# Kernel optimization log

Hardware: AMD Instinct MI355X
Metric: run time of the kernel (lower is better)

Reference implementation:

```python
import jax, jax.numpy as jnp
import numpy as np

N_NODES = 50000
N_EDGES = 800000
D_IN = 128
D_OUT = 128


def setup_inputs() -> dict:
    key = jax.random.key(0)
    k1, k2, k3, k4, k5 = jax.random.split(key, 5)
    gain = float(np.sqrt(2.0))  # calculate_gain('relu')
    # xavier_uniform bound: gain * sqrt(6/(fan_in+fan_out))
    bound = gain * float(np.sqrt(6.0 / (D_IN + D_OUT)))
    feat = jax.random.normal(k1, (N_NODES, D_IN), dtype=jnp.float32)
    weight = jax.random.uniform(k2, (D_IN, D_OUT), minval=-bound, maxval=bound, dtype=jnp.float32)
    loop_weight = jax.random.uniform(k3, (D_IN, D_OUT), minval=-bound, maxval=bound, dtype=jnp.float32)
    h_bias = jnp.zeros((D_OUT,), dtype=jnp.float32)
    src = jax.random.randint(k4, (N_EDGES,), 0, N_NODES, dtype=jnp.int32)
    dst = jax.random.randint(k5, (N_EDGES,), 0, N_NODES, dtype=jnp.int32)
    return {"feat": feat, "weight": weight, "h_bias": h_bias,
            "loop_weight": loop_weight, "src": src, "dst": dst}


def reference(feat, weight, h_bias, loop_weight, src, dst):
    # message: m_e = feat[src_e] @ W ; aggregate: h_v = sum_{e: dst_e=v} m_e
    # (equivalently transform-then-gather, which avoids the [E, D] matmul)
    transformed = feat @ weight                    # [N, D_out]
    msgs = transformed[src]                        # [E, D_out] gather
    h = jax.ops.segment_sum(msgs, dst, num_segments=feat.shape[0])  # [N, D_out]
    h = h + h_bias                                 # bias
    h = h + feat @ loop_weight                     # self-loop
    # activation=None, dropout=0 -> identity
    return h
```

## Files before the change

kernel.cpp:

```cpp
#include <hip/hip_runtime.h>

#define D 128
#define CAP 64
#define FCHUNK 4096

typedef __attribute__((ext_vector_type(8))) short bf16x8;
typedef __attribute__((ext_vector_type(4))) float f32x4;

__device__ inline unsigned short f2bf_rne(float x) {
    unsigned u = __float_as_uint(x);
    return (unsigned short)((u + 0x7FFFu + ((u >> 16) & 1u)) >> 16);
}

__global__ __launch_bounds__(256) void prep_kernel(
    const float* __restrict__ W, const float* __restrict__ LW,
    unsigned short* __restrict__ Bt, int* __restrict__ cursor, int ncur)
{
    int tid = blockIdx.x * 256 + threadIdx.x;
    if (tid < 2 * D * D) {
        int n = tid >> 7;
        int k = tid & 127;
        float v = (n < D) ? W[(size_t)k * D + n] : LW[(size_t)k * D + (n - D)];
        Bt[(size_t)n * D + k] = f2bf_rne(v);
    }
    int j = tid - 2 * D * D;
    if (j >= 0 && j < ncur) cursor[j] = 0;
}

__global__ __launch_bounds__(256) void fill_kernel(
    const int* __restrict__ src, const int* __restrict__ dst,
    int* __restrict__ cursor, unsigned short* __restrict__ ebuf,
    int E, int cstride)
{
    const int chunk = blockIdx.x >> 3;
    const int cls   = blockIdx.x & 7;
    const int base  = chunk * FCHUNK;

    for (int i = threadIdx.x; i < FCHUNK; i += 256) {
        const int e = base + i;
        if (e >= E) break;
        const int d = dst[e];
        const int s = src[e];
        if ((d & 7) == cls) {
            int pos = atomicAdd(&cursor[(cls * cstride) + (d >> 3)], 1);
            if (pos < CAP) ebuf[(size_t)d * CAP + pos] = (unsigned short)s;
        }
    }
}

__global__ __launch_bounds__(256) void mfma_transform(
    const float* __restrict__ feat, const unsigned short* __restrict__ Bt,
    unsigned short* __restrict__ T2, int N)
{
    const int wave = threadIdx.x >> 6;
    const int lane = threadIdx.x & 63;
    const int wrow0 = blockIdx.x * 64 + wave * 16;
    const int m    = lane & 15;
    const int kg   = lane >> 4;

    int arow_idx = wrow0 + m;
    if (arow_idx >= N) arow_idx = N - 1;
    const float* arow = feat + (size_t)arow_idx * D;

    bf16x8 a[4];
#pragma unroll
    for (int ks = 0; ks < 4; ++ks) {
        const float4 f0 = *(const float4*)(arow + ks * 32 + kg * 8);
        const float4 f1 = *(const float4*)(arow + ks * 32 + kg * 8 + 4);
        bf16x8 v;
        v[0] = (short)f2bf_rne(f0.x); v[1] = (short)f2bf_rne(f0.y);
        v[2] = (short)f2bf_rne(f0.z); v[3] = (short)f2bf_rne(f0.w);
        v[4] = (short)f2bf_rne(f1.x); v[5] = (short)f2bf_rne(f1.y);
        v[6] = (short)f2bf_rne(f1.z); v[7] = (short)f2bf_rne(f1.w);
        a[ks] = v;
    }

    f32x4 acc[16];
#pragma unroll
    for (int t = 0; t < 16; ++t) acc[t] = (f32x4){0.f, 0.f, 0.f, 0.f};

#pragma unroll
    for (int t = 0; t < 16; ++t) {
        const unsigned short* brow = Bt + (size_t)(t * 16 + m) * D;
        bf16x8 b0 = *(const bf16x8*)(brow + 0 * 32 + kg * 8);
        bf16x8 b1 = *(const bf16x8*)(brow + 1 * 32 + kg * 8);
        bf16x8 b2 = *(const bf16x8*)(brow + 2 * 32 + kg * 8);
        bf16x8 b3 = *(const bf16x8*)(brow + 3 * 32 + kg * 8);
        acc[t] = __builtin_amdgcn_mfma_f32_16x16x32_bf16(a[0], b0, acc[t], 0, 0, 0);
        acc[t] = __builtin_amdgcn_mfma_f32_16x16x32_bf16(a[1], b1, acc[t], 0, 0, 0);
        acc[t] = __builtin_amdgcn_mfma_f32_16x16x32_bf16(a[2], b2, acc[t], 0, 0, 0);
        acc[t] = __builtin_amdgcn_mfma_f32_16x16x32_bf16(a[3], b3, acc[t], 0, 0, 0);
    }

    const bool full = (wrow0 + 16) <= N;
#pragma unroll
    for (int t = 0; t < 16; ++t) {
        const int col = t * 16 + m;
#pragma unroll
        for (int r = 0; r < 4; ++r) {
            const int row = wrow0 + kg * 4 + r;
            if (full || row < N) T2[(size_t)row * 256 + col] = f2bf_rne(acc[t][r]);
        }
    }
}

__global__ __launch_bounds__(256) void gather_kernel(
    const unsigned short* __restrict__ ebuf, const int* __restrict__ cursor,
    const unsigned short* __restrict__ T2, const float* __restrict__ bias,
    float* __restrict__ out, int N, int cstride)
{
    const int node = (blockIdx.x * 256 + threadIdx.x) >> 6;
    const int lane = threadIdx.x & 63;
    if (node >= N) return;

    int deg = cursor[((node & 7) * cstride) + (node >> 3)];
    if (deg > CAP) deg = CAP;

    const unsigned* region = (const unsigned*)(ebuf + (size_t)node * CAP);
    const unsigned short* Tbase = T2 + 2 * lane;

    float ax = 0.f, ay = 0.f;

    for (int j = 0; j < deg; j += 8) {
        unsigned w[4];
#pragma unroll
        for (int k = 0; k < 4; ++k) w[k] = region[(j >> 1) + k];

        unsigned u[8];
#pragma unroll
        for (int k = 0; k < 8; ++k) {
            const unsigned s = (k & 1) ? (w[k >> 1] >> 16) : (w[k >> 1] & 0xFFFFu);
            u[k] = *(const unsigned*)(Tbase + (size_t)s * 256);
        }
#pragma unroll
        for (int k = 0; k < 8; ++k) {
            const bool live = (j + k) < deg;
            ax += live ? __uint_as_float(u[k] << 16) : 0.f;
            ay += live ? __uint_as_float(u[k] & 0xFFFF0000u) : 0.f;
        }
    }

    const unsigned sw = *(const unsigned*)(T2 + (size_t)node * 256 + 128 + 2 * lane);
    const float2 b = *(const float2*)(bias + 2 * lane);
    float2 o;
    o.x = b.x + __uint_as_float(sw << 16) + ax;
    o.y = b.y + __uint_as_float(sw & 0xFFFF0000u) + ay;
    *(float2*)(out + (size_t)node * D + 2 * lane) = o;
}

extern "C" void kernel_launch(void* const* d_in, const int* in_sizes, int n_in,
                              void* d_out, int out_size, void* d_ws, size_t ws_size,
                              hipStream_t stream) {
    const float* feat = (const float*)d_in[0];
    const float* W    = (const float*)d_in[1];
    const float* bias = (const float*)d_in[2];
    const float* LW   = (const float*)d_in[3];
    const int*   src  = (const int*)d_in[4];
    const int*   dst  = (const int*)d_in[5];
    float* out = (float*)d_out;

    const int N = in_sizes[0] / D;
    const int E = in_sizes[4];
    const int cstride = (N + 7) >> 3;
    const int ncur = 8 * cstride;

    unsigned short* T2   = (unsigned short*)d_ws;
    unsigned short* Bt   = T2 + (size_t)N * 256;
    unsigned short* ebuf = Bt + 2 * D * D;
    int* cursor = (int*)(ebuf + (size_t)N * CAP);

    {
        const int work = 2 * D * D + ncur;
        prep_kernel<<<dim3((work + 255) / 256), 256, 0, stream>>>(W, LW, Bt, cursor, ncur);
    }

    {
        const int nchunks = (E + FCHUNK - 1) / FCHUNK;
        fill_kernel<<<dim3(nchunks * 8), 256, 0, stream>>>(src, dst, cursor, ebuf, E, cstride);
    }

    mfma_transform<<<dim3((N + 63) / 64), 256, 0, stream>>>(feat, Bt, T2, N);

    gather_kernel<<<dim3((N + 3) / 4), 256, 0, stream>>>(ebuf, cursor, T2, bias, out, N, cstride);
}
```

Baseline: 189.0 us.

## Stage MFMA output through LDS and split gather wave across two edges

```diff
diff --git a/kernel.cpp b/kernel.cpp
--- a/kernel.cpp
+++ b/kernel.cpp
@@ -3,6 +3,7 @@
 #define D 128
 #define CAP 64
 #define FCHUNK 4096
+#define LROW 264
 
 typedef __attribute__((ext_vector_type(8))) short bf16x8;
 typedef __attribute__((ext_vector_type(4))) float f32x4;
@@ -11,6 +12,8 @@
     unsigned u = __float_as_uint(x);
     return (unsigned short)((u + 0x7FFFu + ((u >> 16) & 1u)) >> 16);
 }
+__device__ inline float bf_lo(unsigned u) { return __uint_as_float(u << 16); }
+__device__ inline float bf_hi(unsigned u) { return __uint_as_float(u & 0xFFFF0000u); }
 
 __global__ __launch_bounds__(256) void prep_kernel(
     const float* __restrict__ W, const float* __restrict__ LW,
@@ -52,6 +55,7 @@
     const float* __restrict__ feat, const unsigned short* __restrict__ Bt,
     unsigned short* __restrict__ T2, int N)
 {
+    __shared__ unsigned short tile[4 * 16 * LROW];
     const int wave = threadIdx.x >> 6;
     const int lane = threadIdx.x & 63;
     const int wrow0 = blockIdx.x * 64 + wave * 16;
@@ -92,14 +96,23 @@
         acc[t] = __builtin_amdgcn_mfma_f32_16x16x32_bf16(a[3], b3, acc[t], 0, 0, 0);
     }
 
-    const bool full = (wrow0 + 16) <= N;
+    unsigned short* wtile = tile + wave * 16 * LROW;
 #pragma unroll
     for (int t = 0; t < 16; ++t) {
-        const int col = t * 16 + m;
-#pragma unroll
-        for (int r = 0; r < 4; ++r) {
-            const int row = wrow0 + kg * 4 + r;
-            if (full || row < N) T2[(size_t)row * 256 + col] = f2bf_rne(acc[t][r]);
+#pragma unroll
+        for (int r = 0; r < 4; ++r)
+            wtile[(kg * 4 + r) * LROW + t * 16 + m] = f2bf_rne(acc[t][r]);
+    }
+    __syncthreads();
+
+#pragma unroll
+    for (int i = 0; i < 8; ++i) {
+        const int f   = i * 64 + lane;
+        const int row = f >> 5;
+        const int cs  = f & 31;
+        if (wrow0 + row < N) {
+            const uint4 v = *(const uint4*)(wtile + row * LROW + cs * 8);
+            *(uint4*)(T2 + (size_t)(wrow0 + row) * 256 + cs * 8) = v;
         }
     }
 }
@@ -113,39 +126,50 @@
     const int lane = threadIdx.x & 63;
     if (node >= N) return;
 
+    const int h = lane >> 5;
+    const int q = lane & 31;
+
     int deg = cursor[((node & 7) * cstride) + (node >> 3)];
     if (deg > CAP) deg = CAP;
 
     const unsigned* region = (const unsigned*)(ebuf + (size_t)node * CAP);
-    const unsigned short* Tbase = T2 + 2 * lane;
-
-    float ax = 0.f, ay = 0.f;
-
-    for (int j = 0; j < deg; j += 8) {
-        unsigned w[4];
-#pragma unroll
-        for (int k = 0; k < 4; ++k) w[k] = region[(j >> 1) + k];
-
-        unsigned u[8];
+    const unsigned short* Tq = T2 + q * 4;
+
+    float a0 = 0.f, a1 = 0.f, a2 = 0.f, a3 = 0.f;
+
+    for (int j = 0; j < deg; j += 16) {
+        uint2 u[8];
 #pragma unroll
         for (int k = 0; k < 8; ++k) {
-            const unsigned s = (k & 1) ? (w[k >> 1] >> 16) : (w[k >> 1] & 0xFFFFu);
-            u[k] = *(const unsigned*)(Tbase + (size_t)s * 256);
+            const unsigned w = region[(j >> 1) + k];
+            const unsigned s = h ? (w >> 16) : (w & 0xFFFFu);
+            u[k] = *(const uint2*)(Tq + (size_t)s * 256);
         }
 #pragma unroll
         for (int k = 0; k < 8; ++k) {
-            const bool live = (j + k) < deg;
-            ax += live ? __uint_as_float(u[k] << 16) : 0.f;
-            ay += live ? __uint_as_float(u[k] & 0xFFFF0000u) : 0.f;
-        }
-    }
-
-    const unsigned sw = *(const unsigned*)(T2 + (size_t)node * 256 + 128 + 2 * lane);
-    const float2 b = *(const float2*)(bias + 2 * lane);
-    float2 o;
-    o.x = b.x + __uint_as_float(sw << 16) + ax;
-    o.y = b.y + __uint_as_float(sw & 0xFFFF0000u) + ay;
-    *(float2*)(out + (size_t)node * D + 2 * lane) = o;
+            const bool live = (j + 2 * k + h) < deg;
+            a0 += live ? bf_lo(u[k].x) : 0.f;
+            a1 += live ? bf_hi(u[k].x) : 0.f;
+            a2 += live ? bf_lo(u[k].y) : 0.f;
+            a3 += live ? bf_hi(u[k].y) : 0.f;
+        }
+    }
+
+    a0 += __shfl_xor(a0, 32, 64);
+    a1 += __shfl_xor(a1, 32, 64);
+    a2 += __shfl_xor(a2, 32, 64);
+    a3 += __shfl_xor(a3, 32, 64);
+
+    if (h == 0) {
+        const uint2 sv = *(const uint2*)(T2 + (size_t)node * 256 + 128 + q * 4);
+        const float4 b = *(const float4*)(bias + q * 4);
+        float4 o;
+        o.x = b.x + bf_lo(sv.x) + a0;
+        o.y = b.y + bf_hi(sv.x) + a1;
+        o.z = b.z + bf_lo(sv.y) + a2;
+        o.w = b.w + bf_hi(sv.y) + a3;
+        *(float4*)(out + (size_t)node * D + q * 4) = o;
+    }
 }
 
 extern "C" void kernel_launch(void* const* d_in, const int* in_sizes, int n_in,
```

Result: no change. 188.8 us (-0.1%).
